# Kernel optimization log

Measured on AMD Instinct MI355X. Metric: run time of the kernel, lower is better.

The kernel has to match this reference:

```python
import jax, jax.numpy as jnp
import numpy as np

B, T, D, H = 4, 4096, 256, 64  # batch, seq, DIM_EMBEDDING (fixed constant), head_size


def setup_inputs() -> dict:
    key = jax.random.key(0)
    ks = jax.random.split(key, 6)
    x = jax.random.normal(ks[0], (B, T, D), dtype=jnp.float32)
    scale = jnp.float32(0.02)
    Wq = jax.random.normal(ks[1], (D, H), dtype=jnp.float32) * scale
    Wk = jax.random.normal(ks[2], (D, H), dtype=jnp.float32) * scale
    Wv = jax.random.normal(ks[3], (D, H), dtype=jnp.float32) * scale
    two_pi = jnp.float32(2.0 * np.pi)
    angles_x = jax.random.uniform(ks[4], (T, H // 4), dtype=jnp.float32, maxval=two_pi)
    angles_y = jax.random.uniform(ks[5], (T, H // 4), dtype=jnp.float32, maxval=two_pi)
    return {"x": x, "Wq": Wq, "Wk": Wk, "Wv": Wv, "angles_x": angles_x, "angles_y": angles_y}


def _rope_half(v, freqs):
    # v: (B, T, H/2) real; freqs: (T, H/4) complex64 (unit phasors)
    b, t, h = v.shape
    vc = v.astype(jnp.float32).reshape(b, t, h // 2, 2)
    vz = jax.lax.complex(vc[..., 0], vc[..., 1])         # (B, T, H/4)
    rz = vz * freqs[None]                                 # complex multiply per position
    out = jnp.stack([jnp.real(rz), jnp.imag(rz)], axis=-1)
    return out.reshape(b, t, h)


def _rope2d(v, fx, fy):
    vx, vy = jnp.split(v, 2, axis=-1)
    return jnp.concatenate([_rope_half(vx, fx), _rope_half(vy, fy)], axis=-1)


def reference(x, Wq, Wk, Wv, angles_x, angles_y):
    # complex unit phasors e^{i*theta}
    fx = jax.lax.complex(jnp.cos(angles_x), jnp.sin(angles_x))
    fy = jax.lax.complex(jnp.cos(angles_y), jnp.sin(angles_y))
    # original apply_rotary_embeddings is wrapped in @torch.no_grad -> detached
    q = jax.lax.stop_gradient(_rope2d(x @ Wq, fx, fy))
    k = jax.lax.stop_gradient(_rope2d(x @ Wk, fx, fy))
    v = x @ Wv
    C = x.shape[-1]  # NOTE: source scales by embedding dim (256), not head dim
    wei = jnp.einsum('bth,bsh->bts', q, k) / jnp.sqrt(jnp.float32(C))
    softwei = jax.nn.softmax(wei, axis=-1)  # no causal mask in source
    out = jnp.einsum('bts,bsh->bth', softwei, v)
    return out
```

## Files before the change

### kernel.cpp

```cpp
#include <hip/hip_runtime.h>

#define B_ 4
#define T_ 4096
#define D_ 256
#define H_ 64
#define NBT (B_ * T_)
#define NBTH (B_ * T_ * H_)

typedef __bf16 bf16x8 __attribute__((ext_vector_type(8)));
typedef float f32x4 __attribute__((ext_vector_type(4)));

__device__ __forceinline__ unsigned short f2bf(float f) {
  union { float f; unsigned int u; } v; v.f = f;
  unsigned int u = v.u;
  return (unsigned short)((u + 0x7fffu + ((u >> 16) & 1u)) >> 16);
}

#if __has_builtin(__builtin_amdgcn_cvt_pk_bf16_f32)
typedef __bf16 bf16x2_t __attribute__((ext_vector_type(2)));
__device__ __forceinline__ unsigned int pk2(float a, float b) {
  union { bf16x2_t v; unsigned int u; } c;
  c.v = __builtin_amdgcn_cvt_pk_bf16_f32(a, b);
  return c.u;
}
#else
__device__ __forceinline__ unsigned int pk2(float a, float b) {
  return (unsigned int)f2bf(a) | ((unsigned int)f2bf(b) << 16);
}
#endif

#if __has_builtin(__builtin_amdgcn_exp2f)
#define EXP2(x) __builtin_amdgcn_exp2f(x)
#else
#define EXP2(x) exp2f(x)
#endif

#define QSCALE 0.09016844f


__global__ __launch_bounds__(256) void prep_w_kernel(
    const float* __restrict__ Wq, const float* __restrict__ Wk,
    const float* __restrict__ Wv, unsigned short* __restrict__ wt) {
  const int m = blockIdx.x >> 2;
  const int cp = blockIdx.x & 3;
  const float* W = (m == 0) ? Wq : (m == 1) ? Wk : Wv;
  const float scale = (m == 0) ? QSCALE : 1.f;
  __shared__ __align__(16) unsigned short tile[64][72];
  int h = threadIdx.x & 63, dq = threadIdx.x >> 6;
  const int d0 = cp * 64;
  for (int dl = dq; dl < 64; dl += 4)
    tile[h][dl] = f2bf(W[(d0 + dl) * H_ + h] * scale);
  __syncthreads();
  int ht = threadIdx.x >> 6;
  int lane = threadIdx.x & 63, quad = lane >> 4, l16 = lane & 15;
#pragma unroll
  for (int cl = 0; cl < 2; ++cl) {
    int c = cp * 2 + cl;
    bf16x8 v = *(const bf16x8*)&tile[ht * 16 + l16][cl * 32 + quad * 8];
    *(bf16x8*)&wt[(((m * 4 + ht) * 8 + c) << 9) + lane * 8] = v;
  }
}

__global__ __launch_bounds__(192) void qkv_kernel(
    const float* __restrict__ x, const unsigned short* __restrict__ wt,
    const float* __restrict__ axg, const float* __restrict__ ayg,
    unsigned short* __restrict__ qo, unsigned short* __restrict__ ko,
    unsigned short* __restrict__ vt) {
  const int row0g = blockIdx.x * 16;
  const int tid = threadIdx.x;
  const int w = tid / 64, lane = tid & 63, quad = lane >> 4, l16 = lane & 15;

  __shared__ unsigned short xs[16][264];
  __shared__ unsigned short qkt[2][16][72];
  __shared__ unsigned short vsh[64][16];

  const float4* xb = (const float4*)(x + (size_t)row0g * D_);
  for (int i = tid; i < 1024; i += 192) {
    float4 v = xb[i];
    int r = i >> 6, c4 = (i & 63) << 2;
    *(unsigned int*)&xs[r][c4] = pk2(v.x, v.y);
    *(unsigned int*)&xs[r][c4 + 2] = pk2(v.z, v.w);
  }
  __syncthreads();

  bf16x8 xf[8];
#pragma unroll
  for (int c = 0; c < 8; ++c)
    xf[c] = *(const bf16x8*)&xs[l16][c * 32 + quad * 8];

  const unsigned short* wb = wt + (((size_t)w * 4) * 8 << 9);
  f32x4 acc[4];
#pragma unroll
  for (int ht = 0; ht < 4; ++ht) acc[ht] = (f32x4){0.f, 0.f, 0.f, 0.f};
#pragma unroll
  for (int c = 0; c < 8; ++c) {
#pragma unroll
    for (int ht = 0; ht < 4; ++ht) {
      bf16x8 wf = *(const bf16x8*)&wb[((ht * 8 + c) << 9) + lane * 8];
      acc[ht] = __builtin_amdgcn_mfma_f32_16x16x32_bf16(xf[c], wf, acc[ht],
                                                        0, 0, 0);
    }
  }

  const int row0loc = row0g & (T_ - 1);
  if (w < 2) {
    const float sgn = (l16 & 1) ? 1.f : -1.f;
#pragma unroll
    for (int ht = 0; ht < 4; ++ht) {
      int hh = ht * 16 + l16;
      int pidx = (hh & 31) >> 1;
      const float* ab = (hh >= 32) ? ayg : axg;
#pragma unroll
      for (int r = 0; r < 4; ++r) {
        int t = row0loc + quad * 4 + r;
        float s, c;
        __sincosf(ab[t * 16 + pidx], &s, &c);
        float val = acc[ht][r];
        float par = __shfl_xor(val, 1);
        qkt[w][quad * 4 + r][hh] = f2bf(val * c + sgn * par * s);
      }
    }
    asm volatile("s_waitcnt lgkmcnt(0)" ::: "memory");
    unsigned short* dst;
    size_t base;
    if (w == 0) {
      dst = qo;
      base = ((size_t)(row0g >> 4) * 2) << 9;
    } else {
      dst = ko;
      base = ((size_t)((row0g >> 6) * 8 + ((row0g >> 4) & 3) * 2)) << 9;
    }
#pragma unroll
    for (int half = 0; half < 2; ++half) {
      bf16x8 v = *(const bf16x8*)&qkt[w][l16][half * 32 + quad * 8];
      *(bf16x8*)&dst[base + half * 512 + lane * 8] = v;
    }
  } else {
#pragma unroll
    for (int ht = 0; ht < 4; ++ht)
#pragma unroll
      for (int r = 0; r < 4; ++r)
        vsh[ht * 16 + l16][quad * 4 + r] = f2bf(acc[ht][r]);
    asm volatile("s_waitcnt lgkmcnt(0)" ::: "memory");
    const int kvblk = row0g >> 6;
    const int mt = (row0g >> 4) & 3;
    const int half_v = mt >> 1, qlow = (mt & 1) * 2;
#pragma unroll
    for (int it = 0; it < 2; ++it) {
      int hhx = it * 2 + (quad >> 1);
      int qp = qlow + (quad & 1);
      bf16x8 v = *(const bf16x8*)&vsh[hhx * 16 + l16][(quad & 1) * 8];
      *(bf16x8*)&vt[((((size_t)kvblk * 4 + hhx) * 2 + half_v) << 9) +
                    (qp * 16 + l16) * 8] = v;
    }
  }
}

#define LDP 72

__global__ __launch_bounds__(256, 2) void attn_kernel(
    const unsigned short* __restrict__ qfg, const unsigned short* __restrict__ kfg,
    const unsigned short* __restrict__ vfg, float* __restrict__ opart,
    float* __restrict__ lpart, int kv_len) {
  const int split = blockIdx.x >> 6;
  const int rem = blockIdx.x & 63;
  const int b = rem >> 4;
  const int q0 = (rem & 15) * 256;
  const int tid = threadIdx.x;
  const int w = tid >> 6, lane = tid & 63, quad = lane >> 4, l16 = lane & 15;

  __shared__ unsigned short Ps[4][64 * LDP];

  bf16x8 qf[4][2];
#pragma unroll
  for (int u = 0; u < 4; ++u) {
    size_t rb = (size_t)(b * T_ + q0 + w * 64 + u * 16) >> 4;
#pragma unroll
    for (int half = 0; half < 2; ++half)
      qf[u][half] = *(const bf16x8*)&qfg[((rb * 2 + half) << 9) + lane * 8];
  }

  f32x4 oacc[4][4];
  float lsum[4] = {0.f, 0.f, 0.f, 0.f};
  const f32x4 vzero = {0.f, 0.f, 0.f, 0.f};
#pragma unroll
  for (int u = 0; u < 4; ++u)
#pragma unroll
    for (int hh = 0; hh < 4; ++hh) oacc[u][hh] = vzero;

  const int kvb0 = (b * T_ + split * kv_len) >> 6;
  const int nkvb = kv_len >> 6;

  bf16x8 kf[8];
  {
    const unsigned short* kfb = kfg + ((size_t)kvb0 << 12);
#pragma unroll
    for (int f = 0; f < 8; ++f)
      kf[f] = *(const bf16x8*)&kfb[(f << 9) + lane * 8];
  }

  for (int kb = 0; kb < nkvb; ++kb) {
    const unsigned short* vfb = vfg + ((size_t)(kvb0 + kb) << 12);
    const int kbn = (kb + 1 < nkvb) ? (kb + 1) : kb;
    const unsigned short* kfb_n = kfg + ((size_t)(kvb0 + kbn) << 12);

#pragma unroll
    for (int mt = 0; mt < 4; ++mt) {
#pragma unroll
      for (int u = 0; u < 4; ++u) {
        f32x4 s = vzero;
        s = __builtin_amdgcn_mfma_f32_16x16x32_bf16(kf[mt * 2 + 0], qf[u][0],
                                                    s, 0, 0, 0);
        s = __builtin_amdgcn_mfma_f32_16x16x32_bf16(kf[mt * 2 + 1], qf[u][1],
                                                    s, 0, 0, 0);
        float p0 = EXP2(s[0]);
        float p1 = EXP2(s[1]);
        float p2 = EXP2(s[2]);
        float p3 = EXP2(s[3]);
        lsum[u] += (p0 + p1) + (p2 + p3);
        uint2 pk;
        pk.x = pk2(p0, p1);
        pk.y = pk2(p2, p3);
        *(uint2*)&Ps[w][(u * 16 + l16) * LDP + mt * 16 + quad * 4] = pk;
      }
    }

    bf16x8 vf[8];
#pragma unroll
    for (int f = 0; f < 8; ++f)
      vf[f] = *(const bf16x8*)&vfb[(f << 9) + lane * 8];
#pragma unroll
    for (int f = 0; f < 8; ++f)
      kf[f] = *(const bf16x8*)&kfb_n[(f << 9) + lane * 8];

    asm volatile("s_waitcnt lgkmcnt(0)" ::: "memory");

    bf16x8 ap[4][2];
#pragma unroll
    for (int u = 0; u < 4; ++u)
#pragma unroll
      for (int half = 0; half < 2; ++half)
        ap[u][half] =
            *(const bf16x8*)&Ps[w][(u * 16 + l16) * LDP + half * 32 + quad * 8];

#pragma unroll
    for (int hh = 0; hh < 4; ++hh) {
#pragma unroll
      for (int u = 0; u < 4; ++u) {
        oacc[u][hh] = __builtin_amdgcn_mfma_f32_16x16x32_bf16(
            ap[u][0], vf[hh * 2 + 0], oacc[u][hh], 0, 0, 0);
        oacc[u][hh] = __builtin_amdgcn_mfma_f32_16x16x32_bf16(
            ap[u][1], vf[hh * 2 + 1], oacc[u][hh], 0, 0, 0);
      }
    }
  }

#pragma unroll
  for (int u = 0; u < 4; ++u) {
    size_t base = (size_t)(split * B_ + b) * T_ + q0 + w * 64 + u * 16;
#pragma unroll
    for (int r = 0; r < 4; ++r) {
      float* orow = opart + (base + quad * 4 + r) * H_;
#pragma unroll
      for (int hh = 0; hh < 4; ++hh) orow[hh * 16 + l16] = oacc[u][hh][r];
    }
    float l = lsum[u];
    l += __shfl_xor(l, 16);
    l += __shfl_xor(l, 32);
    if (quad == 0) lpart[base + l16] = l;
  }
}

__global__ __launch_bounds__(256) void combine_kernel(
    const float* __restrict__ opart, const float* __restrict__ lpart,
    float* __restrict__ out, int ns) {
  int idx = blockIdx.x * 256 + threadIdx.x;
  int bt = idx >> 4;
  float den = 0.f;
  float axx = 0.f, ayy = 0.f, azz = 0.f, aww = 0.f;
  for (int s = 0; s < ns; ++s) {
    den += lpart[s * NBT + bt];
    float4 o = ((const float4*)opart)[(size_t)s * (NBTH / 4) + idx];
    axx += o.x; ayy += o.y; azz += o.z; aww += o.w;
  }
  float inv = 1.f / den;
  float4 res;
  res.x = axx * inv; res.y = ayy * inv; res.z = azz * inv; res.w = aww * inv;
  ((float4*)out)[idx] = res;
}

extern "C" void kernel_launch(void* const* d_in, const int* in_sizes, int n_in,
                              void* d_out, int out_size, void* d_ws,
                              size_t ws_size, hipStream_t stream) {
  const float* x  = (const float*)d_in[0];
  const float* Wq = (const float*)d_in[1];
  const float* Wk = (const float*)d_in[2];
  const float* Wv = (const float*)d_in[3];
  const float* ax = (const float*)d_in[4];
  const float* ay = (const float*)d_in[5];
  float* out = (float*)d_out;

  unsigned short* qo = (unsigned short*)d_ws;
  unsigned short* ko = qo + NBTH;
  unsigned short* vt = ko + NBTH;
  unsigned short* wt = vt + NBTH;
  float* opart = (float*)(wt + 3 * H_ * D_);

  size_t fixed = (size_t)3 * NBTH * 2 + (size_t)3 * H_ * D_ * 2;
  int NS = (ws_size >= fixed + (size_t)8 * NBTH * 4 + (size_t)8 * NBT * 4 + 256)
               ? 8 : 4;
  float* lpart = opart + (size_t)NS * NBTH;

  prep_w_kernel<<<12, 256, 0, stream>>>(Wq, Wk, Wv, wt);
  qkv_kernel<<<NBT / 16, 192, 0, stream>>>(x, wt, ax, ay, qo, ko, vt);
  attn_kernel<<<NS * 64, 256, 0, stream>>>(qo, ko, vt, opart, lpart, T_ / NS);
  combine_kernel<<<NBTH / 4 / 256, 256, 0, stream>>>(opart, lpart, out, NS);
}
```

Baseline: 110.8 us.

## Stage K/V tiles into LDS via async loads and fuse combine into attention

Replaces per-wave register loads of K and V fragments with double-buffered global_load_lds staging shared by all four waves, synchronised with barriers and vmcnt waits. It also removes the separate combine kernel: each attention block increments an atomic counter per query tile, and the last split block reduces the partial outputs and denominators into the final output. The counters are zeroed in prep_w_kernel. This cuts a kernel launch and redundant global K/V fetches per wave, at the cost of extra LDS (lower occupancy risk), added barriers, and a serialized tail reduction done by one block per tile.

```diff
diff --git a/kernel.cpp b/kernel.cpp
--- a/kernel.cpp
+++ b/kernel.cpp
@@ -37,10 +37,18 @@
 
 #define QSCALE 0.09016844f
 
+__device__ __forceinline__ void gload_lds16(const void* g, void* l) {
+  __builtin_amdgcn_global_load_lds(
+      (__attribute__((address_space(1))) void*)(g),
+      (__attribute__((address_space(3))) void*)(l), 16, 0, 0);
+}
+
 
 __global__ __launch_bounds__(256) void prep_w_kernel(
     const float* __restrict__ Wq, const float* __restrict__ Wk,
-    const float* __restrict__ Wv, unsigned short* __restrict__ wt) {
+    const float* __restrict__ Wv, unsigned short* __restrict__ wt,
+    int* __restrict__ cnt) {
+  if (blockIdx.x == 0 && threadIdx.x < 64) cnt[threadIdx.x] = 0;
   const int m = blockIdx.x >> 2;
   const int cp = blockIdx.x & 3;
   const float* W = (m == 0) ? Wq : (m == 1) ? Wk : Wv;
@@ -161,7 +169,8 @@
 __global__ __launch_bounds__(256, 2) void attn_kernel(
     const unsigned short* __restrict__ qfg, const unsigned short* __restrict__ kfg,
     const unsigned short* __restrict__ vfg, float* __restrict__ opart,
-    float* __restrict__ lpart, int kv_len) {
+    float* __restrict__ lpart, int* __restrict__ cnt, float* __restrict__ out,
+    int kv_len) {
   const int split = blockIdx.x >> 6;
   const int rem = blockIdx.x & 63;
   const int b = rem >> 4;
@@ -169,7 +178,10 @@
   const int tid = threadIdx.x;
   const int w = tid >> 6, lane = tid & 63, quad = lane >> 4, l16 = lane & 15;
 
+  __shared__ __align__(16) unsigned short Kbuf[2][4096];
+  __shared__ __align__(16) unsigned short Vbuf[2][4096];
   __shared__ unsigned short Ps[4][64 * LDP];
+  __shared__ int last_flag;
 
   bf16x8 qf[4][2];
 #pragma unroll
@@ -179,6 +191,23 @@
     for (int half = 0; half < 2; ++half)
       qf[u][half] = *(const bf16x8*)&qfg[((rb * 2 + half) << 9) + lane * 8];
   }
+
+  const int kvb0 = (b * T_ + split * kv_len) >> 6;
+  const int nkvb = kv_len >> 6;
+
+  auto stage = [&](int kb, int buf) {
+    const unsigned short* kfb = kfg + ((size_t)(kvb0 + kb) << 12);
+    const unsigned short* vfb = vfg + ((size_t)(kvb0 + kb) << 12);
+#pragma unroll
+    for (int i = 0; i < 2; ++i) {
+      int f = w * 2 + i;
+      gload_lds16(kfb + (f << 9) + lane * 8, &Kbuf[buf][f * 512]);
+      gload_lds16(vfb + (f << 9) + lane * 8, &Vbuf[buf][f * 512]);
+    }
+  };
+
+  stage(0, 0);
+  if (nkvb > 1) stage(1, 1);
 
   f32x4 oacc[4][4];
   float lsum[4] = {0.f, 0.f, 0.f, 0.f};
@@ -188,31 +217,23 @@
 #pragma unroll
     for (int hh = 0; hh < 4; ++hh) oacc[u][hh] = vzero;
 
-  const int kvb0 = (b * T_ + split * kv_len) >> 6;
-  const int nkvb = kv_len >> 6;
-
-  bf16x8 kf[8];
-  {
-    const unsigned short* kfb = kfg + ((size_t)kvb0 << 12);
-#pragma unroll
-    for (int f = 0; f < 8; ++f)
-      kf[f] = *(const bf16x8*)&kfb[(f << 9) + lane * 8];
-  }
-
   for (int kb = 0; kb < nkvb; ++kb) {
-    const unsigned short* vfb = vfg + ((size_t)(kvb0 + kb) << 12);
-    const int kbn = (kb + 1 < nkvb) ? (kb + 1) : kb;
-    const unsigned short* kfb_n = kfg + ((size_t)(kvb0 + kbn) << 12);
+    const int cur = kb & 1;
+    if (kb + 1 < nkvb) asm volatile("s_waitcnt vmcnt(4)" ::: "memory");
+    else               asm volatile("s_waitcnt vmcnt(0)" ::: "memory");
+    __builtin_amdgcn_sched_barrier(0);
+    __builtin_amdgcn_s_barrier();
+    __builtin_amdgcn_sched_barrier(0);
 
 #pragma unroll
     for (int mt = 0; mt < 4; ++mt) {
+      bf16x8 k0 = *(const bf16x8*)&Kbuf[cur][(mt * 2 + 0) * 512 + lane * 8];
+      bf16x8 k1 = *(const bf16x8*)&Kbuf[cur][(mt * 2 + 1) * 512 + lane * 8];
 #pragma unroll
       for (int u = 0; u < 4; ++u) {
         f32x4 s = vzero;
-        s = __builtin_amdgcn_mfma_f32_16x16x32_bf16(kf[mt * 2 + 0], qf[u][0],
-                                                    s, 0, 0, 0);
-        s = __builtin_amdgcn_mfma_f32_16x16x32_bf16(kf[mt * 2 + 1], qf[u][1],
-                                                    s, 0, 0, 0);
+        s = __builtin_amdgcn_mfma_f32_16x16x32_bf16(k0, qf[u][0], s, 0, 0, 0);
+        s = __builtin_amdgcn_mfma_f32_16x16x32_bf16(k1, qf[u][1], s, 0, 0, 0);
         float p0 = EXP2(s[0]);
         float p1 = EXP2(s[1]);
         float p2 = EXP2(s[2]);
@@ -224,15 +245,6 @@
         *(uint2*)&Ps[w][(u * 16 + l16) * LDP + mt * 16 + quad * 4] = pk;
       }
     }
-
-    bf16x8 vf[8];
-#pragma unroll
-    for (int f = 0; f < 8; ++f)
-      vf[f] = *(const bf16x8*)&vfb[(f << 9) + lane * 8];
-#pragma unroll
-    for (int f = 0; f < 8; ++f)
-      kf[f] = *(const bf16x8*)&kfb_n[(f << 9) + lane * 8];
-
     asm volatile("s_waitcnt lgkmcnt(0)" ::: "memory");
 
     bf16x8 ap[4][2];
@@ -242,15 +254,24 @@
       for (int half = 0; half < 2; ++half)
         ap[u][half] =
             *(const bf16x8*)&Ps[w][(u * 16 + l16) * LDP + half * 32 + quad * 8];
+    bf16x8 vr[8];
+#pragma unroll
+    for (int f = 0; f < 8; ++f)
+      vr[f] = *(const bf16x8*)&Vbuf[cur][f * 512 + lane * 8];
+    asm volatile("s_waitcnt lgkmcnt(0)" ::: "memory");
+    __builtin_amdgcn_sched_barrier(0);
+    __builtin_amdgcn_s_barrier();
+    __builtin_amdgcn_sched_barrier(0);
+    if (kb + 2 < nkvb) stage(kb + 2, cur);
 
 #pragma unroll
     for (int hh = 0; hh < 4; ++hh) {
 #pragma unroll
       for (int u = 0; u < 4; ++u) {
         oacc[u][hh] = __builtin_amdgcn_mfma_f32_16x16x32_bf16(
-            ap[u][0], vf[hh * 2 + 0], oacc[u][hh], 0, 0, 0);
+            ap[u][0], vr[hh * 2 + 0], oacc[u][hh], 0, 0, 0);
         oacc[u][hh] = __builtin_amdgcn_mfma_f32_16x16x32_bf16(
-            ap[u][1], vf[hh * 2 + 1], oacc[u][hh], 0, 0, 0);
+            ap[u][1], vr[hh * 2 + 1], oacc[u][hh], 0, 0, 0);
       }
     }
   }
@@ -269,24 +290,32 @@
     l += __shfl_xor(l, 32);
     if (quad == 0) lpart[base + l16] = l;
   }
-}
-
-__global__ __launch_bounds__(256) void combine_kernel(
-    const float* __restrict__ opart, const float* __restrict__ lpart,
-    float* __restrict__ out, int ns) {
-  int idx = blockIdx.x * 256 + threadIdx.x;
-  int bt = idx >> 4;
-  float den = 0.f;
-  float axx = 0.f, ayy = 0.f, azz = 0.f, aww = 0.f;
-  for (int s = 0; s < ns; ++s) {
-    den += lpart[s * NBT + bt];
-    float4 o = ((const float4*)opart)[(size_t)s * (NBTH / 4) + idx];
-    axx += o.x; ayy += o.y; azz += o.z; aww += o.w;
-  }
-  float inv = 1.f / den;
-  float4 res;
-  res.x = axx * inv; res.y = ayy * inv; res.z = azz * inv; res.w = aww * inv;
-  ((float4*)out)[idx] = res;
+
+  __threadfence();
+  if (tid == 0) {
+    int old = atomicAdd(&cnt[rem], 1);
+    last_flag = (old == (int)(gridDim.x >> 6) - 1);
+  }
+  __syncthreads();
+  if (last_flag) {
+    __threadfence();
+    const int ns = gridDim.x >> 6;
+    for (int i = tid; i < 256 * 16; i += 256) {
+      int r = i >> 4, h4 = i & 15;
+      size_t row = (size_t)b * T_ + q0 + r;
+      float den = 0.f;
+      float ax = 0.f, ay = 0.f, az = 0.f, aw = 0.f;
+      for (int s = 0; s < ns; ++s) {
+        den += lpart[(size_t)s * NBT + row];
+        float4 o = *(const float4*)&opart[((size_t)s * NBT + row) * H_ + h4 * 4];
+        ax += o.x; ay += o.y; az += o.z; aw += o.w;
+      }
+      float inv = 1.f / den;
+      float4 res;
+      res.x = ax * inv; res.y = ay * inv; res.z = az * inv; res.w = aw * inv;
+      *(float4*)&out[row * H_ + h4 * 4] = res;
+    }
+  }
 }
 
 extern "C" void kernel_launch(void* const* d_in, const int* in_sizes, int n_in,
@@ -307,12 +336,13 @@
   float* opart = (float*)(wt + 3 * H_ * D_);
 
   size_t fixed = (size_t)3 * NBTH * 2 + (size_t)3 * H_ * D_ * 2;
-  int NS = (ws_size >= fixed + (size_t)8 * NBTH * 4 + (size_t)8 * NBT * 4 + 256)
+  int NS = (ws_size >= fixed + (size_t)8 * NBTH * 4 + (size_t)8 * NBT * 4 + 512)
                ? 8 : 4;
   float* lpart = opart + (size_t)NS * NBTH;
-
-  prep_w_kernel<<<12, 256, 0, stream>>>(Wq, Wk, Wv, wt);
+  int* cnt = (int*)(lpart + (size_t)NS * NBT);
+
+  prep_w_kernel<<<12, 256, 0, stream>>>(Wq, Wk, Wv, wt, cnt);
   qkv_kernel<<<NBT / 16, 192, 0, stream>>>(x, wt, ax, ay, qo, ko, vt);
-  attn_kernel<<<NS * 64, 256, 0, stream>>>(qo, ko, vt, opart, lpart, T_ / NS);
-  combine_kernel<<<NBTH / 4 / 256, 256, 0, stream>>>(opart, lpart, out, NS);
-}
+  attn_kernel<<<NS * 64, 256, 0, stream>>>(qo, ko, vt, opart, lpart, cnt, out,
+                                           T_ / NS);
+}
```

Result: slower. 209.6 us (+89.1%).

## Fuse split-KV combine into attention kernel via last-block atomic counter

Applied to the files above, without the earlier changes.

Removes the separate combine kernel launch. Each attention block bumps a per-tile atomic counter after writing its partial output, and the last split block to finish for that query tile reduces all partials and writes the final output. The counters are zeroed in the weight-prep kernel. This saves one launch and its gap, but the reduction now runs serially in a few tail blocks with strided float4 reads, and it adds threadfence and atomic overhead.

```diff
diff --git a/kernel.cpp b/kernel.cpp
--- a/kernel.cpp
+++ b/kernel.cpp
@@ -40,7 +40,9 @@
 
 __global__ __launch_bounds__(256) void prep_w_kernel(
     const float* __restrict__ Wq, const float* __restrict__ Wk,
-    const float* __restrict__ Wv, unsigned short* __restrict__ wt) {
+    const float* __restrict__ Wv, unsigned short* __restrict__ wt,
+    int* __restrict__ cnt) {
+  if (blockIdx.x == 0 && threadIdx.x < 64) cnt[threadIdx.x] = 0;
   const int m = blockIdx.x >> 2;
   const int cp = blockIdx.x & 3;
   const float* W = (m == 0) ? Wq : (m == 1) ? Wk : Wv;
@@ -161,7 +163,8 @@
 __global__ __launch_bounds__(256, 2) void attn_kernel(
     const unsigned short* __restrict__ qfg, const unsigned short* __restrict__ kfg,
     const unsigned short* __restrict__ vfg, float* __restrict__ opart,
-    float* __restrict__ lpart, int kv_len) {
+    float* __restrict__ lpart, int* __restrict__ cnt, float* __restrict__ out,
+    int kv_len) {
   const int split = blockIdx.x >> 6;
   const int rem = blockIdx.x & 63;
   const int b = rem >> 4;
@@ -170,6 +173,7 @@
   const int w = tid >> 6, lane = tid & 63, quad = lane >> 4, l16 = lane & 15;
 
   __shared__ unsigned short Ps[4][64 * LDP];
+  __shared__ int last_flag;
 
   bf16x8 qf[4][2];
 #pragma unroll
@@ -269,24 +273,32 @@
     l += __shfl_xor(l, 32);
     if (quad == 0) lpart[base + l16] = l;
   }
-}
-
-__global__ __launch_bounds__(256) void combine_kernel(
-    const float* __restrict__ opart, const float* __restrict__ lpart,
-    float* __restrict__ out, int ns) {
-  int idx = blockIdx.x * 256 + threadIdx.x;
-  int bt = idx >> 4;
-  float den = 0.f;
-  float axx = 0.f, ayy = 0.f, azz = 0.f, aww = 0.f;
-  for (int s = 0; s < ns; ++s) {
-    den += lpart[s * NBT + bt];
-    float4 o = ((const float4*)opart)[(size_t)s * (NBTH / 4) + idx];
-    axx += o.x; ayy += o.y; azz += o.z; aww += o.w;
-  }
-  float inv = 1.f / den;
-  float4 res;
-  res.x = axx * inv; res.y = ayy * inv; res.z = azz * inv; res.w = aww * inv;
-  ((float4*)out)[idx] = res;
+
+  __threadfence();
+  if (tid == 0) {
+    int old = atomicAdd(&cnt[rem], 1);
+    last_flag = (old == (int)(gridDim.x >> 6) - 1);
+  }
+  __syncthreads();
+  if (last_flag) {
+    __threadfence();
+    const int ns = gridDim.x >> 6;
+    for (int i = tid; i < 256 * 16; i += 256) {
+      int r = i >> 4, h4 = i & 15;
+      size_t row = (size_t)b * T_ + q0 + r;
+      float den = 0.f;
+      float ax = 0.f, ay = 0.f, az = 0.f, aw = 0.f;
+      for (int s = 0; s < ns; ++s) {
+        den += lpart[(size_t)s * NBT + row];
+        float4 o = *(const float4*)&opart[((size_t)s * NBT + row) * H_ + h4 * 4];
+        ax += o.x; ay += o.y; az += o.z; aw += o.w;
+      }
+      float inv = 1.f / den;
+      float4 res;
+      res.x = ax * inv; res.y = ay * inv; res.z = az * inv; res.w = aw * inv;
+      *(float4*)&out[row * H_ + h4 * 4] = res;
+    }
+  }
 }
 
 extern "C" void kernel_launch(void* const* d_in, const int* in_sizes, int n_in,
@@ -307,12 +319,13 @@
   float* opart = (float*)(wt + 3 * H_ * D_);
 
   size_t fixed = (size_t)3 * NBTH * 2 + (size_t)3 * H_ * D_ * 2;
-  int NS = (ws_size >= fixed + (size_t)8 * NBTH * 4 + (size_t)8 * NBT * 4 + 256)
+  int NS = (ws_size >= fixed + (size_t)8 * NBTH * 4 + (size_t)8 * NBT * 4 + 512)
                ? 8 : 4;
   float* lpart = opart + (size_t)NS * NBTH;
-
-  prep_w_kernel<<<12, 256, 0, stream>>>(Wq, Wk, Wv, wt);
+  int* cnt = (int*)(lpart + (size_t)NS * NBT);
+
+  prep_w_kernel<<<12, 256, 0, stream>>>(Wq, Wk, Wv, wt, cnt);
   qkv_kernel<<<NBT / 16, 192, 0, stream>>>(x, wt, ax, ay, qo, ko, vt);
-  attn_kernel<<<NS * 64, 256, 0, stream>>>(qo, ko, vt, opart, lpart, T_ / NS);
-  combine_kernel<<<NBTH / 4 / 256, 256, 0, stream>>>(opart, lpart, out, NS);
-}
+  attn_kernel<<<NS * 64, 256, 0, stream>>>(qo, ko, vt, opart, lpart, cnt, out,
+                                           T_ / NS);
+}
```

After: 216.7 us. 95.5% more time.
